# Kernel tuning notes

Hardware: AMD Instinct MI355X
Metric: run time of the kernel (lower is better)

Reference implementation:

```python
import jax, jax.numpy as jnp
import numpy as np

H = 10  # hidden_dim

def _lstm_layer(x_tbd, w_ih, w_hh, b_ih, b_hh):
    # x_tbd: [T, B, D]; w_ih: [4H, D]; w_hh: [4H, H]; biases [4H]
    B = x_tbd.shape[1]
    h0 = jnp.zeros((B, H), x_tbd.dtype)
    c0 = jnp.zeros((B, H), x_tbd.dtype)
    # precompute input projections for all timesteps: [T, B, 4H]
    xg = jnp.einsum('tbd,gd->tbg', x_tbd, w_ih) + b_ih + b_hh

    def step(carry, xg_t):
        h, c = carry
        gates = xg_t + h @ w_hh.T  # [B, 4H]
        i, f, g, o = jnp.split(gates, 4, axis=-1)  # torch gate order i,f,g,o
        i = jax.nn.sigmoid(i); f = jax.nn.sigmoid(f)
        g = jnp.tanh(g); o = jax.nn.sigmoid(o)
        c = f * c + i * g
        h = o * jnp.tanh(c)
        return (h, c), h

    (hT, cT), hs = jax.lax.scan(step, (h0, c0), xg)
    return hs, hT  # hs: [T, B, H]

def setup_inputs() -> dict:
    key = jax.random.key(0)
    ks = jax.random.split(key, 11)
    B, T, D = 32768, 28, 28
    s0 = 1.0 / np.sqrt(H)
    u = lambda k, shape: jax.random.uniform(k, shape, jnp.float32, -s0, s0)
    return {
        'x': jax.random.normal(ks[0], (B, T, D), jnp.float32),
        'w_ih0': u(ks[1], (4 * H, D)),
        'w_hh0': u(ks[2], (4 * H, H)),
        'b_ih0': u(ks[3], (4 * H,)),
        'b_hh0': u(ks[4], (4 * H,)),
        'w_ih1': u(ks[5], (4 * H, H)),
        'w_hh1': u(ks[6], (4 * H, H)),
        'b_ih1': u(ks[7], (4 * H,)),
        'b_hh1': u(ks[8], (4 * H,)),
        'w_cls': u(ks[9], (10, H)),
        'b_cls': u(ks[10], (10,)),
    }

def reference(x, w_ih0, w_hh0, b_ih0, b_hh0, w_ih1, w_hh1, b_ih1, b_hh1, w_cls, b_cls):
    x_tbd = jnp.swapaxes(x, 0, 1)  # [T, B, D]
    hs0, _ = _lstm_layer(x_tbd, w_ih0, w_hh0, b_ih0, b_hh0)
    _, hT1 = _lstm_layer(hs0, w_ih1, w_hh1, b_ih1, b_hh1)  # hT1 = h_n[-1]
    return hT1 @ w_cls.T + b_cls  # [B, 10]
```

## Files before the change

### kernel.cpp

```cpp
#include <hip/hip_runtime.h>


#define HDIM 10
#define DDIM 28
#define TSTEPS 28
#define NX 14

typedef __attribute__((ext_vector_type(8))) short short8;
typedef __attribute__((ext_vector_type(4))) float f32x4;

__device__ __forceinline__ unsigned short bf16_rne(float f) {
    unsigned u = __builtin_bit_cast(unsigned, f);
    u += 0x7FFFu + ((u >> 16) & 1u);
    return (unsigned short)(u >> 16);
}
__device__ __forceinline__ float bf16_f(unsigned short h) {
    unsigned u = ((unsigned)h) << 16;
    return __builtin_bit_cast(float, u);
}
__device__ __forceinline__ unsigned pk_hl(float v) {
    unsigned a, p;
    const float z = 0.0f;
    asm("v_cvt_pk_bf16_f32 %0, %1, %2" : "=v"(a) : "v"(v), "v"(z));
    const float hif = __builtin_bit_cast(float, a << 16);
    const float d = v - hif;
    asm("v_cvt_pk_bf16_f32 %0, %1, %2" : "=v"(p) : "v"(v), "v"(d));
    return p;
}
__device__ __forceinline__ float sig_f(float v) {
    return __builtin_amdgcn_rcpf(1.0f + __expf(-v));
}
__device__ __forceinline__ float tanh_f(float v) {
    return 2.0f * __builtin_amdgcn_rcpf(1.0f + __expf(-2.0f * v)) - 1.0f;
}

#define FENCE() __asm volatile("" ::: "memory")
#define WR32(arrp, sidx, val) (*(unsigned*)&(arrp)[(sidx)] = (val))

#define BODY(P, Q, T) do {                                                    \
    _Pragma("unroll")                                                         \
    for (int mh = 0; mh < 2; ++mh) {                                          \
        _Pragma("unroll")                                                     \
        for (int c = 0; c < 2; ++c)                                           \
            A1f[mh][c] = *(const short8*)&uA1w[(16 * mh + lm) * 72 + 32 * c + 8 * q]; \
        _Pragma("unroll")                                                     \
        for (int c = 0; c < 4; ++c)                                           \
            A0f[mh][c] = *(const short8*)&uA0w[(16 * mh + lm) * 136 + 32 * c + 8 * q]; \
    }                                                                         \
    FENCE();                                                                  \
    if ((T) < TSTEPS - 3) {                                                   \
        _Pragma("unroll")                                                     \
        for (int i = 0; i < NX; ++i) { xoff[i] += DDIM; Q[i] = x[xoff[i]]; }  \
    }                                                                         \
    f32x4 C[2][4], D[2][4];                                                   \
    _Pragma("unroll")                                                         \
    for (int mh = 0; mh < 2; ++mh) {                                          \
        _Pragma("unroll")                                                     \
        for (int T4 = 0; T4 < 4; ++T4) {                                      \
            f32x4 accD = {bias1[T4], bias1[T4], bias1[T4], bias1[T4]};        \
            _Pragma("unroll")                                                 \
            for (int c = 0; c < 2; ++c)                                       \
                accD = __builtin_amdgcn_mfma_f32_16x16x32_bf16(A1f[mh][c], B1[T4][c], accD, 0, 0, 0); \
            D[mh][T4] = accD;                                                 \
            f32x4 accC = {bias0[T4], bias0[T4], bias0[T4], bias0[T4]};        \
            _Pragma("unroll")                                                 \
            for (int c = 0; c < 4; ++c)                                       \
                accC = __builtin_amdgcn_mfma_f32_16x16x32_bf16(A0f[mh][c], B0[T4][c], accC, 0, 0, 0); \
            C[mh][T4] = accC;                                                 \
        }                                                                     \
    }                                                                         \
    _Pragma("unroll")                                                         \
    for (int mh = 0; mh < 2; ++mh) {                                          \
        _Pragma("unroll")                                                     \
        for (int r = 0; r < 4; ++r) {                                         \
            const float i1 = sig_f(D[mh][0][r]);                              \
            const float f1 = sig_f(D[mh][1][r]);                              \
            const float g1 = tanh_f(D[mh][2][r]);                             \
            const float o1 = sig_f(D[mh][3][r]);                              \
            const float c1 = f1 * c1s[mh][r] + i1 * g1;                       \
            c1s[mh][r] = c1;                                                  \
            h1v[mh][r] = o1 * tanh_f(c1);                                     \
            const float i0 = sig_f(C[mh][0][r]);                              \
            const float f0 = sig_f(C[mh][1][r]);                              \
            const float g0 = tanh_f(C[mh][2][r]);                             \
            const float o0 = sig_f(C[mh][3][r]);                              \
            const float c0 = f0 * c0s[mh][r] + i0 * g0;                       \
            c0s[mh][r] = c0;                                                  \
            h0v[mh][r] = o0 * tanh_f(c0);                                     \
        }                                                                     \
    }                                                                         \
    if ((T) < TSTEPS - 2) {                                                   \
        _Pragma("unroll")                                                     \
        for (int i = 0; i < NX; ++i) {                                        \
            const unsigned p = pk_hl(P[i]);                                   \
            WR32(uA0w, lofsA[i], p);                                          \
            uA0w[lofsB[i]] = (unsigned short)p;                               \
        }                                                                     \
    }                                                                         \
    if (lm < 10) {                                                            \
        _Pragma("unroll")                                                     \
        for (int mh = 0; mh < 2; ++mh) {                                      \
            _Pragma("unroll")                                                 \
            for (int r = 0; r < 4; ++r) {                                     \
                const int m = 16 * mh + 4 * q + r;                            \
                const unsigned p1 = pk_hl(h1v[mh][r]);                        \
                unsigned short* r1 = &uA1w[m * 72];                           \
                WR32(r1, 20 + 2 * lm, p1); r1[50 + lm] = (unsigned short)p1;  \
                const unsigned p0 = pk_hl(h0v[mh][r]);                        \
                WR32(r1, 2 * lm, p0);      r1[40 + lm] = (unsigned short)p0;  \
                unsigned short* r0 = &uA0w[m * 136];                          \
                WR32(r0, 56 + 2 * lm, p0); r0[104 + lm] = (unsigned short)p0; \
            }                                                                 \
        }                                                                     \
    }                                                                         \
    FENCE();                                                                  \
} while (0)

__global__ __launch_bounds__(128, 1) void lstm2_mfma_kernel(
    const float* __restrict__ x,
    const float* __restrict__ w_ih0, const float* __restrict__ w_hh0,
    const float* __restrict__ b_ih0, const float* __restrict__ b_hh0,
    const float* __restrict__ w_ih1, const float* __restrict__ w_hh1,
    const float* __restrict__ b_ih1, const float* __restrict__ b_hh1,
    const float* __restrict__ w_cls, const float* __restrict__ b_cls,
    float* __restrict__ out)
{
    __shared__ __align__(16) unsigned short uA0s[2][32 * 136];
    __shared__ __align__(16) unsigned short uA1s[2][32 * 72];
    __shared__ __align__(16) float hfins[2][32 * 12];

    const int l   = threadIdx.x & 63;
    const int wid = threadIdx.x >> 6;
    const int lm  = l & 15;
    const int q   = l >> 4;
    const int sbase = (blockIdx.x * 2 + wid) * 32;

    unsigned short* const uA0w = uA0s[wid];
    unsigned short* const uA1w = uA1s[wid];
    float* const hfinw = hfins[wid];

    for (int i = l; i < 32 * 22; i += 64) uA0w[(i / 22) * 136 + 114 + (i % 22)] = 0;
    for (int i = l; i < 32 * 12; i += 64) uA1w[(i / 12) * 72 + 60 + (i % 12)] = 0;

    short8 B0[4][4], B1[4][2];
    const bool gvalid = (lm < 10);
    #pragma unroll
    for (int T = 0; T < 4; ++T) {
        const int g = 10 * T + lm;
        #pragma unroll
        for (int c = 0; c < 4; ++c) {
            #pragma unroll
            for (int j = 0; j < 8; ++j) {
                const int kk = 32 * c + 8 * q + j;
                unsigned short bits = 0;
                if (gvalid && kk < 114) {
                    if (kk < 76) {
                        const int j2 = kk >> 1;
                        const float w = (j2 < 28) ? w_ih0[g * 28 + j2]
                                                  : w_hh0[g * 10 + (j2 - 28)];
                        bits = bf16_rne(w);
                    } else {
                        const int d = kk - 76;
                        const float w = (d < 28) ? w_ih0[g * 28 + d]
                                                 : w_hh0[g * 10 + (d - 28)];
                        const unsigned short hi = bf16_rne(w);
                        bits = bf16_rne(w - bf16_f(hi));
                    }
                }
                B0[T][c][j] = (short)bits;
            }
        }
        #pragma unroll
        for (int c = 0; c < 2; ++c) {
            #pragma unroll
            for (int j = 0; j < 8; ++j) {
                const int kk = 32 * c + 8 * q + j;
                unsigned short bits = 0;
                if (gvalid && kk < 60) {
                    if (kk < 40) {
                        const int j2 = kk >> 1;
                        const float w = (j2 < 10) ? w_ih1[g * 10 + j2]
                                                  : w_hh1[g * 10 + (j2 - 10)];
                        bits = bf16_rne(w);
                    } else {
                        const int d = kk - 40;
                        const float w = (d < 10) ? w_ih1[g * 10 + d]
                                                 : w_hh1[g * 10 + (d - 10)];
                        const unsigned short hi = bf16_rne(w);
                        bits = bf16_rne(w - bf16_f(hi));
                    }
                }
                B1[T][c][j] = (short)bits;
            }
        }
    }

    float bias0[4], bias1[4];
    #pragma unroll
    for (int T = 0; T < 4; ++T) {
        const int g = 10 * T + lm;
        bias0[T] = gvalid ? (b_ih0[g] + b_hh0[g]) : 0.0f;
        bias1[T] = gvalid ? (b_ih1[g] + b_hh1[g]) : 0.0f;
    }

    int xoff[NX], lofsA[NX], lofsB[NX];
    float xA[NX], xB[NX];
    #pragma unroll
    for (int i = 0; i < NX; ++i) {
        const int f = l + 64 * i;
        const int sm = f / 28, d = f - 28 * sm;
        lofsA[i] = sm * 136 + 2 * d;
        lofsB[i] = sm * 136 + 76 + d;
        xoff[i] = (sbase + sm) * (TSTEPS * DDIM) + d;
        xA[i] = x[xoff[i]];
    }
    #pragma unroll
    for (int i = 0; i < NX; ++i) {
        const unsigned p = pk_hl(xA[i]);
        WR32(uA0w, lofsA[i], p);
        uA0w[lofsB[i]] = (unsigned short)p;
    }
    if (lm < 10) {
        #pragma unroll
        for (int mh = 0; mh < 2; ++mh) {
            #pragma unroll
            for (int r = 0; r < 4; ++r) {
                const int m = 16 * mh + 4 * q + r;
                unsigned short* r0 = &uA0w[m * 136];
                WR32(r0, 56 + 2 * lm, 0u); r0[104 + lm] = 0;
                unsigned short* r1 = &uA1w[m * 72];
                WR32(r1, 2 * lm, 0u);      r1[40 + lm] = 0;
                WR32(r1, 20 + 2 * lm, 0u); r1[50 + lm] = 0;
            }
        }
    }
    FENCE();

    float c0s[2][4] = {{0,0,0,0},{0,0,0,0}}, c1s[2][4] = {{0,0,0,0},{0,0,0,0}};
    float h1v[2][4] = {{0,0,0,0},{0,0,0,0}};
    float h0v[2][4];
    short8 A0f[2][4], A1f[2][2];

    #pragma unroll
    for (int i = 0; i < NX; ++i) { xoff[i] += DDIM; xA[i] = x[xoff[i]]; }

    #pragma unroll
    for (int mh = 0; mh < 2; ++mh)
        #pragma unroll
        for (int c = 0; c < 4; ++c)
            A0f[mh][c] = *(const short8*)&uA0w[(16 * mh + lm) * 136 + 32 * c + 8 * q];
    FENCE();
    #pragma unroll
    for (int i = 0; i < NX; ++i) { xoff[i] += DDIM; xB[i] = x[xoff[i]]; }
    {
        f32x4 C[2][4];
        #pragma unroll
        for (int mh = 0; mh < 2; ++mh) {
            #pragma unroll
            for (int T = 0; T < 4; ++T) {
                f32x4 acc = {bias0[T], bias0[T], bias0[T], bias0[T]};
                #pragma unroll
                for (int c = 0; c < 4; ++c)
                    acc = __builtin_amdgcn_mfma_f32_16x16x32_bf16(A0f[mh][c], B0[T][c], acc, 0, 0, 0);
                C[mh][T] = acc;
            }
        }
        #pragma unroll
        for (int mh = 0; mh < 2; ++mh) {
            #pragma unroll
            for (int r = 0; r < 4; ++r) {
                const float i0 = sig_f(C[mh][0][r]);
                const float f0 = sig_f(C[mh][1][r]);
                const float g0 = tanh_f(C[mh][2][r]);
                const float o0 = sig_f(C[mh][3][r]);
                const float c0 = f0 * c0s[mh][r] + i0 * g0;
                c0s[mh][r] = c0;
                h0v[mh][r] = o0 * tanh_f(c0);
            }
        }
        if (lm < 10) {
            #pragma unroll
            for (int mh = 0; mh < 2; ++mh) {
                #pragma unroll
                for (int r = 0; r < 4; ++r) {
                    const int m = 16 * mh + 4 * q + r;
                    const unsigned p0 = pk_hl(h0v[mh][r]);
                    unsigned short* r0 = &uA0w[m * 136];
                    WR32(r0, 56 + 2 * lm, p0); r0[104 + lm] = (unsigned short)p0;
                    unsigned short* r1 = &uA1w[m * 72];
                    WR32(r1, 2 * lm, p0);      r1[40 + lm] = (unsigned short)p0;
                }
            }
        }
        #pragma unroll
        for (int i = 0; i < NX; ++i) {
            const unsigned p = pk_hl(xA[i]);
            WR32(uA0w, lofsA[i], p);
            uA0w[lofsB[i]] = (unsigned short)p;
        }
    }
    FENCE();

    #pragma unroll 1
    for (int tp = 0; tp < 13; ++tp) {
        BODY(xB, xA, 2 * tp);
        BODY(xA, xB, 2 * tp + 1);
    }
    BODY(xB, xA, 26);

    {
        #pragma unroll
        for (int mh = 0; mh < 2; ++mh)
            #pragma unroll
            for (int c = 0; c < 2; ++c)
                A1f[mh][c] = *(const short8*)&uA1w[(16 * mh + lm) * 72 + 32 * c + 8 * q];
        FENCE();
        f32x4 D[2][4];
        #pragma unroll
        for (int mh = 0; mh < 2; ++mh) {
            #pragma unroll
            for (int T = 0; T < 4; ++T) {
                f32x4 acc = {bias1[T], bias1[T], bias1[T], bias1[T]};
                #pragma unroll
                for (int c = 0; c < 2; ++c)
                    acc = __builtin_amdgcn_mfma_f32_16x16x32_bf16(A1f[mh][c], B1[T][c], acc, 0, 0, 0);
                D[mh][T] = acc;
            }
        }
        #pragma unroll
        for (int mh = 0; mh < 2; ++mh) {
            #pragma unroll
            for (int r = 0; r < 4; ++r) {
                const float i1 = sig_f(D[mh][0][r]);
                const float f1 = sig_f(D[mh][1][r]);
                const float g1 = tanh_f(D[mh][2][r]);
                const float o1 = sig_f(D[mh][3][r]);
                const float c1 = f1 * c1s[mh][r] + i1 * g1;
                h1v[mh][r] = o1 * tanh_f(c1);
            }
        }
    }

    if (lm < 10) {
        #pragma unroll
        for (int mh = 0; mh < 2; ++mh)
            #pragma unroll
            for (int r = 0; r < 4; ++r)
                hfinw[(16 * mh + 4 * q + r) * 12 + lm] = h1v[mh][r];
    }
    FENCE();
    if (lm < 10) {
        float wc[10];
        #pragma unroll
        for (int j = 0; j < 10; ++j) wc[j] = w_cls[lm * 10 + j];
        const float bo = b_cls[lm];
        #pragma unroll
        for (int mh = 0; mh < 2; ++mh) {
            #pragma unroll
            for (int r = 0; r < 4; ++r) {
                const int m = 16 * mh + 4 * q + r;
                float acc = bo;
                #pragma unroll
                for (int j = 0; j < 10; ++j) acc += hfinw[m * 12 + j] * wc[j];
                out[(size_t)(sbase + m) * 10 + lm] = acc;
            }
        }
    }
}

extern "C" void kernel_launch(void* const* d_in, const int* in_sizes, int n_in,
                              void* d_out, int out_size, void* d_ws, size_t ws_size,
                              hipStream_t stream) {
    const float* x     = (const float*)d_in[0];
    const float* w_ih0 = (const float*)d_in[1];
    const float* w_hh0 = (const float*)d_in[2];
    const float* b_ih0 = (const float*)d_in[3];
    const float* b_hh0 = (const float*)d_in[4];
    const float* w_ih1 = (const float*)d_in[5];
    const float* w_hh1 = (const float*)d_in[6];
    const float* b_ih1 = (const float*)d_in[7];
    const float* b_hh1 = (const float*)d_in[8];
    const float* w_cls = (const float*)d_in[9];
    const float* b_cls = (const float*)d_in[10];
    float* out = (float*)d_out;

    const int B = in_sizes[0] / (TSTEPS * DDIM);
    const int grid = B / 64;

    hipLaunchKernelGGL(lstm2_mfma_kernel, dim3(grid), dim3(128), 0, stream,
                       x, w_ih0, w_hh0, b_ih0, b_hh0,
                       w_ih1, w_hh1, b_ih1, b_hh1,
                       w_cls, b_cls, out);
}
```

Before: 232.9 us.

## Software-pipeline LSTM step across the two row halves to overlap LDS and compute

Splits each timestep body into per-half (mh) phases: read A fragments, compute MFMA plus gates, and write h back to LDS. The writeback of the second half is deferred into the next step, and the second half's LDS reads are issued while the first half's results are being written. This is meant to hide LDS latency and the gate math behind MFMA work. In exchange the control flow gets more complex, the first and last steps need special handling, and register pressure may rise.

```diff
diff --git a/kernel.cpp b/kernel.cpp
--- a/kernel.cpp
+++ b/kernel.cpp
@@ -37,58 +37,81 @@
 #define FENCE() __asm volatile("" ::: "memory")
 #define WR32(arrp, sidx, val) (*(unsigned*)&(arrp)[(sidx)] = (val))
 
-#define BODY(P, Q, T) do {                                                    \
+
+#define RDA(MH) do {                                                          \
     _Pragma("unroll")                                                         \
-    for (int mh = 0; mh < 2; ++mh) {                                          \
+    for (int c = 0; c < 2; ++c)                                               \
+        A1f[MH][c] = *(const short8*)&uA1w[(16 * (MH) + lm) * 72 + 32 * c + 8 * q]; \
+    _Pragma("unroll")                                                         \
+    for (int c = 0; c < 4; ++c)                                               \
+        A0f[MH][c] = *(const short8*)&uA0w[(16 * (MH) + lm) * 136 + 32 * c + 8 * q]; \
+} while (0)
+
+#define CMP(MH) do {                                                          \
+    f32x4 C_[4], D_[4];                                                       \
+    _Pragma("unroll")                                                         \
+    for (int T4 = 0; T4 < 4; ++T4) {                                          \
+        f32x4 accD = {bias1[T4], bias1[T4], bias1[T4], bias1[T4]};            \
         _Pragma("unroll")                                                     \
         for (int c = 0; c < 2; ++c)                                           \
-            A1f[mh][c] = *(const short8*)&uA1w[(16 * mh + lm) * 72 + 32 * c + 8 * q]; \
+            accD = __builtin_amdgcn_mfma_f32_16x16x32_bf16(A1f[MH][c], B1[T4][c], accD, 0, 0, 0); \
+        D_[T4] = accD;                                                        \
+        f32x4 accC = {bias0[T4], bias0[T4], bias0[T4], bias0[T4]};            \
         _Pragma("unroll")                                                     \
         for (int c = 0; c < 4; ++c)                                           \
-            A0f[mh][c] = *(const short8*)&uA0w[(16 * mh + lm) * 136 + 32 * c + 8 * q]; \
+            accC = __builtin_amdgcn_mfma_f32_16x16x32_bf16(A0f[MH][c], B0[T4][c], accC, 0, 0, 0); \
+        C_[T4] = accC;                                                        \
     }                                                                         \
+    _Pragma("unroll")                                                         \
+    for (int r = 0; r < 4; ++r) {                                             \
+        const float i1 = sig_f(D_[0][r]);                                     \
+        const float f1 = sig_f(D_[1][r]);                                     \
+        const float g1 = tanh_f(D_[2][r]);                                    \
+        const float o1 = sig_f(D_[3][r]);                                     \
+        const float c1 = f1 * c1s[MH][r] + i1 * g1;                           \
+        c1s[MH][r] = c1;                                                      \
+        h1v[MH][r] = o1 * tanh_f(c1);                                         \
+        const float i0 = sig_f(C_[0][r]);                                     \
+        const float f0 = sig_f(C_[1][r]);                                     \
+        const float g0 = tanh_f(C_[2][r]);                                    \
+        const float o0 = sig_f(C_[3][r]);                                     \
+        const float c0 = f0 * c0s[MH][r] + i0 * g0;                           \
+        c0s[MH][r] = c0;                                                      \
+        h0v[MH][r] = o0 * tanh_f(c0);                                         \
+    }                                                                         \
+} while (0)
+
+#define WRH(MH) do {                                                          \
+    if (lm < 10) {                                                            \
+        _Pragma("unroll")                                                     \
+        for (int r = 0; r < 4; ++r) {                                         \
+            const int m = 16 * (MH) + 4 * q + r;                              \
+            const unsigned p1 = pk_hl(h1v[MH][r]);                            \
+            unsigned short* r1 = &uA1w[m * 72];                               \
+            WR32(r1, 20 + 2 * lm, p1); r1[50 + lm] = (unsigned short)p1;      \
+            const unsigned p0 = pk_hl(h0v[MH][r]);                            \
+            WR32(r1, 2 * lm, p0);      r1[40 + lm] = (unsigned short)p0;      \
+            unsigned short* r0 = &uA0w[m * 136];                              \
+            WR32(r0, 56 + 2 * lm, p0); r0[104 + lm] = (unsigned short)p0;     \
+        }                                                                     \
+    }                                                                         \
+} while (0)
+
+#define BODY(P, Q, T, FIRST) do {                                             \
+                                    \
+    RDA(0);                                                                   \
+    if (!(FIRST)) { WRH(1); }                                                 \
     FENCE();                                                                  \
+                   \
     if ((T) < TSTEPS - 3) {                                                   \
         _Pragma("unroll")                                                     \
         for (int i = 0; i < NX; ++i) { xoff[i] += DDIM; Q[i] = x[xoff[i]]; }  \
     }                                                                         \
-    f32x4 C[2][4], D[2][4];                                                   \
-    _Pragma("unroll")                                                         \
-    for (int mh = 0; mh < 2; ++mh) {                                          \
-        _Pragma("unroll")                                                     \
-        for (int T4 = 0; T4 < 4; ++T4) {                                      \
-            f32x4 accD = {bias1[T4], bias1[T4], bias1[T4], bias1[T4]};        \
-            _Pragma("unroll")                                                 \
-            for (int c = 0; c < 2; ++c)                                       \
-                accD = __builtin_amdgcn_mfma_f32_16x16x32_bf16(A1f[mh][c], B1[T4][c], accD, 0, 0, 0); \
-            D[mh][T4] = accD;                                                 \
-            f32x4 accC = {bias0[T4], bias0[T4], bias0[T4], bias0[T4]};        \
-            _Pragma("unroll")                                                 \
-            for (int c = 0; c < 4; ++c)                                       \
-                accC = __builtin_amdgcn_mfma_f32_16x16x32_bf16(A0f[mh][c], B0[T4][c], accC, 0, 0, 0); \
-            C[mh][T4] = accC;                                                 \
-        }                                                                     \
-    }                                                                         \
-    _Pragma("unroll")                                                         \
-    for (int mh = 0; mh < 2; ++mh) {                                          \
-        _Pragma("unroll")                                                     \
-        for (int r = 0; r < 4; ++r) {                                         \
-            const float i1 = sig_f(D[mh][0][r]);                              \
-            const float f1 = sig_f(D[mh][1][r]);                              \
-            const float g1 = tanh_f(D[mh][2][r]);                             \
-            const float o1 = sig_f(D[mh][3][r]);                              \
-            const float c1 = f1 * c1s[mh][r] + i1 * g1;                       \
-            c1s[mh][r] = c1;                                                  \
-            h1v[mh][r] = o1 * tanh_f(c1);                                     \
-            const float i0 = sig_f(C[mh][0][r]);                              \
-            const float f0 = sig_f(C[mh][1][r]);                              \
-            const float g0 = tanh_f(C[mh][2][r]);                             \
-            const float o0 = sig_f(C[mh][3][r]);                              \
-            const float c0 = f0 * c0s[mh][r] + i0 * g0;                       \
-            c0s[mh][r] = c0;                                                  \
-            h0v[mh][r] = o0 * tanh_f(c0);                                     \
-        }                                                                     \
-    }                                                                         \
+    CMP(0);                                                                   \
+    RDA(1);                                                                   \
+    FENCE();                                                                  \
+                    \
+    WRH(0);                                                                   \
     if ((T) < TSTEPS - 2) {                                                   \
         _Pragma("unroll")                                                     \
         for (int i = 0; i < NX; ++i) {                                        \
@@ -97,22 +120,7 @@
             uA0w[lofsB[i]] = (unsigned short)p;                               \
         }                                                                     \
     }                                                                         \
-    if (lm < 10) {                                                            \
-        _Pragma("unroll")                                                     \
-        for (int mh = 0; mh < 2; ++mh) {                                      \
-            _Pragma("unroll")                                                 \
-            for (int r = 0; r < 4; ++r) {                                     \
-                const int m = 16 * mh + 4 * q + r;                            \
-                const unsigned p1 = pk_hl(h1v[mh][r]);                        \
-                unsigned short* r1 = &uA1w[m * 72];                           \
-                WR32(r1, 20 + 2 * lm, p1); r1[50 + lm] = (unsigned short)p1;  \
-                const unsigned p0 = pk_hl(h0v[mh][r]);                        \
-                WR32(r1, 2 * lm, p0);      r1[40 + lm] = (unsigned short)p0;  \
-                unsigned short* r0 = &uA0w[m * 136];                          \
-                WR32(r0, 56 + 2 * lm, p0); r0[104 + lm] = (unsigned short)p0; \
-            }                                                                 \
-        }                                                                     \
-    }                                                                         \
+    CMP(1);                                                                   \
     FENCE();                                                                  \
 } while (0)
 
@@ -301,12 +309,17 @@
     }
     FENCE();
 
+    BODY(xB, xA, 0, 1);
+    BODY(xA, xB, 1, 0);
     #pragma unroll 1
-    for (int tp = 0; tp < 13; ++tp) {
-        BODY(xB, xA, 2 * tp);
-        BODY(xA, xB, 2 * tp + 1);
-    }
-    BODY(xB, xA, 26);
+    for (int tp = 1; tp < 13; ++tp) {
+        BODY(xB, xA, 2 * tp, 0);
+        BODY(xA, xB, 2 * tp + 1, 0);
+    }
+    BODY(xB, xA, 26, 0);
+
+    WRH(1);
+    FENCE();
 
     {
         #pragma unroll
```

Result: no change. 236.0 us (+1.3%).
